# Kernel optimization log

Measured on AMD Instinct MI355X. Metric: run time of the kernel, lower is better.

Reference implementation:

```python
import jax, jax.numpy as jnp
import numpy as np

B, DC, DB, DF = 16384, 2048, 768, 256
NF = DB  # num_features (isSwinT=True)
EPS = 1e-5


def setup_inputs() -> dict:
    key = jax.random.key(0)
    ks = jax.random.split(key, 20)
    s = 0.02
    return {
        'x_context': jax.random.normal(ks[0], (B, DC), jnp.float32),
        'x_body': jax.random.normal(ks[1], (B, DB), jnp.float32),
        'x_face': jax.random.normal(ks[2], (B, DF), jnp.float32),
        'Wc': jax.random.normal(ks[3], (NF, DC), jnp.float32) * s,
        'bc': jax.random.normal(ks[4], (NF,), jnp.float32) * s,
        'Wa1': jax.random.normal(ks[5], (128, NF), jnp.float32) * s,
        'ba1': jax.random.normal(ks[6], (128,), jnp.float32) * s,
        'ga': jnp.ones((128,), jnp.float32),
        'bba': jnp.zeros((128,), jnp.float32),
        'Wa2': jax.random.normal(ks[7], (1, 128), jnp.float32) * s,
        'ba2': jax.random.normal(ks[8], (1,), jnp.float32) * s,
        'W1': jax.random.normal(ks[9], (256, NF * 3), jnp.float32) * s,
        'b1': jax.random.normal(ks[10], (256,), jnp.float32) * s,
        'g1': jnp.ones((256,), jnp.float32),
        'be1': jnp.zeros((256,), jnp.float32),
        'Wcat': jax.random.normal(ks[11], (26, 256), jnp.float32) * s,
        'bcat': jax.random.normal(ks[12], (26,), jnp.float32) * s,
    }


def _bn(x, g, b):
    # BatchNorm1d, training mode (biased batch stats), deterministic
    m = jnp.mean(x, axis=0)
    v = jnp.mean((x - m) ** 2, axis=0)
    return (x - m) * jax.lax.rsqrt(v + EPS) * g + b


def reference(x_context, x_body, x_face, Wc, bc, Wa1, ba1, ga, bba, Wa2, ba2,
              W1, b1, g1, be1, Wcat, bcat):
    # face repeated elementwise to body width: [B,256,1]->repeat(3)->view[B,768]
    face = jnp.repeat(x_face, DB // DF, axis=1)              # [B, NF]
    ctx = x_context @ Wc.T + bc                              # [B, NF]
    body = x_body                                            # [B, NF]

    def cross_atten(a, u, v):
        # two 1x1 dot-products, softmax over size-2 dim, weighted sum
        d = jnp.stack([jnp.sum(a * u, axis=1), jnp.sum(a * v, axis=1)], axis=1)  # [B,2]
        att = jax.nn.softmax(d, axis=1)
        # sum over dim2 of a[:, :, None] @ att[:, None, :] == a * att.sum(1)
        return a * jnp.sum(att, axis=1, keepdims=True)

    cfeat = cross_atten(ctx, body, face)
    bfeat = cross_atten(body, ctx, face)
    ffeat = cross_atten(face, ctx, body)

    def fc_att(x):
        h = _bn(x @ Wa1.T + ba1, ga, bba)
        h = jax.nn.gelu(h, approximate=False)
        return h @ Wa2.T + ba2                               # [B, 1]

    score = jax.nn.softmax(
        jnp.concatenate([fc_att(cfeat), fc_att(bfeat), fc_att(ffeat)], axis=1), axis=1)  # [B,3]
    cfeat = cfeat * score[:, 0:1]
    bfeat = bfeat * score[:, 1:2]
    ffeat = ffeat * score[:, 2:3]

    fuse = jnp.concatenate([cfeat, bfeat, ffeat], axis=1) @ W1.T + b1  # [B,256]
    fuse = jax.nn.relu(_bn(fuse, g1, be1))  # dropout p=0.5 treated as identity (eval)
    return fuse @ Wcat.T + bcat             # [B,26]
```

## Files before the change

### kernel.cpp

```cpp
#include <hip/hip_runtime.h>
#include <stdint.h>

typedef float f32x4 __attribute__((ext_vector_type(4)));
typedef short bf16x8 __attribute__((ext_vector_type(8)));
typedef unsigned short u16;

static constexpr int kB  = 16384;
static constexpr int kDC = 2048;
static constexpr int kNF = 768;
static constexpr float kEps = 1e-5f;

static constexpr size_t OFF_FEATS  = 0;
static constexpr size_t OFF_AXBF   = 75497472;
static constexpr size_t OFF_WCBF   = OFF_AXBF + 67108864;
static constexpr size_t OFF_WA1BF  = OFF_WCBF + 3145728;
static constexpr size_t OFF_W1BF   = OFF_WA1BF + 196608;
static constexpr size_t OFF_FUSE   = OFF_W1BF + 1179648;
static constexpr size_t OFF_SCORES = OFF_FUSE + 16777216;
static constexpr size_t OFF_STATS  = OFF_SCORES + 196608;

static __device__ __forceinline__ u16 f2bf(float x) {
  union { float f; unsigned u; } c; c.f = x;
  unsigned r = c.u + 0x7fffu + ((c.u >> 16) & 1u);
  return (u16)(r >> 16);
}

static __device__ __forceinline__ void cvt4(const float* __restrict__ in, u16* __restrict__ out, long v) {
  const float4 f = ((const float4*)in)[v];
  ((ushort4*)out)[v] = make_ushort4(f2bf(f.x), f2bf(f.y), f2bf(f.z), f2bf(f.w));
}

__global__ __launch_bounds__(256) void prep_kernel(
    const float* __restrict__ xc, const float* __restrict__ xb, const float* __restrict__ xf,
    const float* __restrict__ Wc, const float* __restrict__ Wa1, const float* __restrict__ W1,
    u16* __restrict__ axbf, u16* __restrict__ feats,
    u16* __restrict__ wcbf, u16* __restrict__ wa1bf, u16* __restrict__ w1bf)
{
  const int b = blockIdx.x, t = threadIdx.x;
  if (b < 1024) {
    const long base = (long)b * (32 * 256) + t;
#pragma unroll 8
    for (int i = 0; i < 32; ++i) cvt4(xc, axbf, base + (long)i * 256);
  } else if (b < 1536) {
    const long base = (long)(b - 1024) * (24 * 256) + t;
    u16* o = feats + (size_t)kB * kNF;
#pragma unroll 8
    for (int i = 0; i < 24; ++i) cvt4(xb, o, base + (long)i * 256);
  } else if (b < 1792) {
    const long base = (long)(b - 1536) * (16 * 256) + t;
#pragma unroll 4
    for (int i = 0; i < 16; ++i) {
      const long v = base + (long)i * 256;
      const float4 f = ((const float4*)xf)[v];
      u16 e0 = f2bf(f.x), e1 = f2bf(f.y), e2 = f2bf(f.z), e3 = f2bf(f.w);
      size_t p = (size_t)v * 4;
      size_t row = p >> 8;
      int col = (int)(p & 255);
      u16* o = feats + (size_t)2 * kB * kNF + row * kNF + col * 3;
      ushort4* o4 = (ushort4*)o;
      o4[0] = make_ushort4(e0, e0, e0, e1);
      o4[1] = make_ushort4(e1, e1, e2, e2);
      o4[2] = make_ushort4(e2, e3, e3, e3);
    }
  } else if (b < 1888) {
    const long base = (long)(b - 1792) * (16 * 256) + t;
#pragma unroll 8
    for (int i = 0; i < 16; ++i) cvt4(Wc, wcbf, base + (long)i * 256);
  } else if (b < 1896) {
    const long base = (long)(b - 1888) * (12 * 256) + t;
#pragma unroll 4
    for (int i = 0; i < 12; ++i) cvt4(Wa1, wa1bf, base + (long)i * 256);
  } else {
    const long base = (long)(b - 1896) * (18 * 256) + t;
#pragma unroll 6
    for (int i = 0; i < 18; ++i) cvt4(W1, w1bf, base + (long)i * 256);
  }
}

static __device__ __forceinline__ void gload16(const void* g, void* l) {
  __builtin_amdgcn_global_load_lds(
      (const __attribute__((address_space(1))) void*)g,
      (__attribute__((address_space(3))) void*)l, 16, 0, 0);
}

template <int OUT_BF16, int STATS>
__global__ __launch_bounds__(256) void gemm_bt(
    const u16* __restrict__ A, int lda, const u16* __restrict__ B, int ldb,
    const float* __restrict__ bias, void* __restrict__ Cv, int ldc, int K,
    float* __restrict__ stats)
{
  __shared__ __align__(16) u16 As[128 * 32];
  __shared__ __align__(16) u16 Bs[128 * 32];
  const int bx = blockIdx.x, by = blockIdx.y;
  const size_t m0 = (size_t)bx * 128;
  const int n0 = by * 128;
  const int t = threadIdx.x;
  const int lane = t & 63, wave = t >> 6;
  const int wm = (wave >> 1) * 64, wn = (wave & 1) * 64;
  const int fr = lane & 15, fq = lane >> 4;

  const int srow = t >> 2;
  const int scol = (t & 3) * 8;
  const u16* ga0 = A + (m0 + srow) * (size_t)lda + scol;
  const u16* ga1 = A + (m0 + 64 + srow) * (size_t)lda + scol;
  const u16* gb0 = B + (size_t)(n0 + srow) * ldb + scol;
  const u16* gb1 = B + (size_t)(n0 + 64 + srow) * ldb + scol;
  u16* la = As + t * 8;
  u16* lb = Bs + t * 8;
  const u16* fa = As + (wm + fr) * 32 + fq * 8;
  const u16* fb = Bs + (wn + fr) * 32 + fq * 8;

  f32x4 acc[4][4] = {};

  const int kt = K >> 5;
  for (int k = 0; k < kt; ++k) {
    __syncthreads();
    gload16(ga0, la);
    gload16(ga1, la + 2048);
    gload16(gb0, lb);
    gload16(gb1, lb + 2048);
    ga0 += 32; ga1 += 32; gb0 += 32; gb1 += 32;
    __syncthreads();
    bf16x8 av[4], bv[4];
#pragma unroll
    for (int mf = 0; mf < 4; ++mf) av[mf] = *(const bf16x8*)(fa + mf * 512);
#pragma unroll
    for (int nf = 0; nf < 4; ++nf) bv[nf] = *(const bf16x8*)(fb + nf * 512);
#pragma unroll
    for (int mf = 0; mf < 4; ++mf)
#pragma unroll
      for (int nf = 0; nf < 4; ++nf)
        acc[mf][nf] = __builtin_amdgcn_mfma_f32_16x16x32_bf16(av[mf], bv[nf], acc[mf][nf], 0, 0, 0);
  }

  float cs[4] = {}, cs2[4] = {};
#pragma unroll
  for (int mf = 0; mf < 4; ++mf) {
    const size_t rb = m0 + wm + mf * 16 + fq * 4;
#pragma unroll
    for (int nf = 0; nf < 4; ++nf) {
      const int gn = n0 + wn + nf * 16 + fr;
      const float bb = bias ? bias[gn] : 0.0f;
#pragma unroll
      for (int rr = 0; rr < 4; ++rr) {
        const float vv = acc[mf][nf][rr] + bb;
        if (OUT_BF16) ((u16*)Cv)[(rb + rr) * (size_t)ldc + gn] = f2bf(vv);
        else ((float*)Cv)[(rb + rr) * (size_t)ldc + gn] = vv;
        if (STATS) { cs[nf] += vv; cs2[nf] += vv * vv; }
      }
    }
  }
  if (STATS) {
    const int f = (int)(m0 >> 14);
#pragma unroll
    for (int nf = 0; nf < 4; ++nf) {
      float s = cs[nf], s2 = cs2[nf];
      s += __shfl_down(s, 32); s2 += __shfl_down(s2, 32);
      s += __shfl_down(s, 16); s2 += __shfl_down(s2, 16);
      if (fq == 0) {
        const int gn = n0 + wn + nf * 16 + fr;
        atomicAdd(&stats[(f * 128 + gn) * 2 + 0], s);
        atomicAdd(&stats[(f * 128 + gn) * 2 + 1], s2);
      }
    }
  }
}

__global__ __launch_bounds__(256, 2) void gemm_fuse(
    const u16* __restrict__ feats, const u16* __restrict__ w1,
    const float* __restrict__ scores, const float* __restrict__ b1,
    float* __restrict__ fuse, float* __restrict__ fstats)
{
  __shared__ __align__(16) u16 As[128 * 32];
  __shared__ __align__(16) u16 Bs[128 * 32];
  const int bx = blockIdx.x, by = blockIdx.y;
  const int m0 = bx * 128;
  const int n0 = by * 128;
  const int t = threadIdx.x;
  const int lane = t & 63, wave = t >> 6;
  const int wm = (wave >> 1) * 64, wn = (wave & 1) * 64;
  const int fr = lane & 15, fq = lane >> 4;
  const int srow = t >> 2;
  const int scol = (t & 3) * 8;
  u16* la = As + t * 8;
  u16* lb = Bs + t * 8;
  const u16* fa = As + (wm + fr) * 32 + fq * 8;
  const u16* fb = Bs + (wn + fr) * 32 + fq * 8;

  f32x4 tot[4][4] = {};

  for (int f = 0; f < 3; ++f) {
    const u16* ga0 = feats + (size_t)f * kB * kNF + (size_t)(m0 + srow) * kNF + scol;
    const u16* ga1 = ga0 + (size_t)64 * kNF;
    const u16* gb0 = w1 + f * kNF + (size_t)(n0 + srow) * (3 * kNF) + scol;
    const u16* gb1 = gb0 + (size_t)64 * (3 * kNF);

    f32x4 acc[4][4] = {};
    for (int k = 0; k < (kNF >> 5); ++k) {
      __syncthreads();
      gload16(ga0, la);
      gload16(ga1, la + 2048);
      gload16(gb0, lb);
      gload16(gb1, lb + 2048);
      ga0 += 32; ga1 += 32; gb0 += 32; gb1 += 32;
      __syncthreads();
      bf16x8 av[4], bv[4];
#pragma unroll
      for (int mf = 0; mf < 4; ++mf) av[mf] = *(const bf16x8*)(fa + mf * 512);
#pragma unroll
      for (int nf = 0; nf < 4; ++nf) bv[nf] = *(const bf16x8*)(fb + nf * 512);
#pragma unroll
      for (int mf = 0; mf < 4; ++mf)
#pragma unroll
        for (int nf = 0; nf < 4; ++nf)
          acc[mf][nf] = __builtin_amdgcn_mfma_f32_16x16x32_bf16(av[mf], bv[nf], acc[mf][nf], 0, 0, 0);
    }
#pragma unroll
    for (int mf = 0; mf < 4; ++mf) {
      const int rb = m0 + wm + mf * 16 + fq * 4;
#pragma unroll
      for (int rr = 0; rr < 4; ++rr) {
        const float sv = scores[(size_t)(rb + rr) * 3 + f];
#pragma unroll
        for (int nf = 0; nf < 4; ++nf) tot[mf][nf][rr] += sv * acc[mf][nf][rr];
      }
    }
  }

  float cs[4] = {}, cs2[4] = {};
#pragma unroll
  for (int mf = 0; mf < 4; ++mf) {
    const int rb = m0 + wm + mf * 16 + fq * 4;
#pragma unroll
    for (int nf = 0; nf < 4; ++nf) {
      const int gn = n0 + wn + nf * 16 + fr;
      const float bb = b1[gn];
#pragma unroll
      for (int rr = 0; rr < 4; ++rr) {
        const float vv = tot[mf][nf][rr] + bb;
        fuse[(size_t)(rb + rr) * 256 + gn] = vv;
        cs[nf] += vv; cs2[nf] += vv * vv;
      }
    }
  }
#pragma unroll
  for (int nf = 0; nf < 4; ++nf) {
    float s = cs[nf], s2 = cs2[nf];
    s += __shfl_down(s, 32); s2 += __shfl_down(s2, 32);
    s += __shfl_down(s, 16); s2 += __shfl_down(s2, 16);
    if (fq == 0) {
      const int gn = n0 + wn + nf * 16 + fr;
      atomicAdd(&fstats[gn * 2 + 0], s);
      atomicAdd(&fstats[gn * 2 + 1], s2);
    }
  }
}

__global__ __launch_bounds__(64) void att_kernel(
    const float* __restrict__ H, const float* __restrict__ stats,
    const float* __restrict__ ga, const float* __restrict__ bba,
    const float* __restrict__ Wa2, const float* __restrict__ ba2,
    float* __restrict__ scores)
{
  const int i = blockIdx.x, l = threadIdx.x;
  float d[3];
#pragma unroll
  for (int f = 0; f < 3; ++f) {
    float part = 0.f;
#pragma unroll
    for (int h = 0; h < 2; ++h) {
      const int c = l + h * 64;
      const float sum = stats[(f * 128 + c) * 2 + 0];
      const float sq  = stats[(f * 128 + c) * 2 + 1];
      const float m = sum * (1.f / kB);
      const float var = sq * (1.f / kB) - m * m;
      const float rs = rsqrtf(var + kEps);
      const float x = H[((size_t)f * kB + i) * 128 + c];
      const float xn = (x - m) * rs * ga[c] + bba[c];
      const float ge = 0.5f * xn * (1.f + erff(xn * 0.70710678118f));
      part += ge * Wa2[c];
    }
#pragma unroll
    for (int off = 32; off > 0; off >>= 1) part += __shfl_down(part, off);
    d[f] = part;
  }
  if (l == 0) {
    const float b2 = ba2[0];
    float d0 = d[0] + b2, d1 = d[1] + b2, d2 = d[2] + b2;
    const float mx = fmaxf(d0, fmaxf(d1, d2));
    const float e0 = expf(d0 - mx), e1 = expf(d1 - mx), e2 = expf(d2 - mx);
    const float inv = 1.f / (e0 + e1 + e2);
    scores[i * 3 + 0] = e0 * inv;
    scores[i * 3 + 1] = e1 * inv;
    scores[i * 3 + 2] = e2 * inv;
  }
}

__global__ __launch_bounds__(64) void final_kernel(
    const float* __restrict__ fuse, const float* __restrict__ fstats,
    const float* __restrict__ g1, const float* __restrict__ be1,
    const float* __restrict__ Wcat, const float* __restrict__ bcat,
    float* __restrict__ out)
{
  const int i = blockIdx.x, l = threadIdx.x;
  __shared__ float row[256];
#pragma unroll
  for (int h = 0; h < 4; ++h) {
    const int c = l + h * 64;
    const float sum = fstats[c * 2 + 0], sq = fstats[c * 2 + 1];
    const float m = sum * (1.f / kB);
    const float var = sq * (1.f / kB) - m * m;
    const float rs = rsqrtf(var + kEps);
    const float v = (fuse[(size_t)i * 256 + c] - m) * rs * g1[c] + be1[c];
    row[c] = fmaxf(v, 0.f);
  }
  __syncthreads();
  if (l < 26) {
    float acc = bcat[l];
    const float* w = Wcat + l * 256;
    for (int k2 = 0; k2 < 256; ++k2) acc += row[k2] * w[k2];
    out[(size_t)i * 26 + l] = acc;
  }
}

extern "C" void kernel_launch(void* const* d_in, const int* in_sizes, int n_in,
                              void* d_out, int out_size, void* d_ws, size_t ws_size,
                              hipStream_t stream) {
  (void)in_sizes; (void)n_in; (void)out_size; (void)ws_size;
  const float* xc   = (const float*)d_in[0];
  const float* xb   = (const float*)d_in[1];
  const float* xf   = (const float*)d_in[2];
  const float* Wc   = (const float*)d_in[3];
  const float* bc   = (const float*)d_in[4];
  const float* Wa1  = (const float*)d_in[5];
  const float* ba1  = (const float*)d_in[6];
  const float* ga   = (const float*)d_in[7];
  const float* bba  = (const float*)d_in[8];
  const float* Wa2  = (const float*)d_in[9];
  const float* ba2  = (const float*)d_in[10];
  const float* W1   = (const float*)d_in[11];
  const float* b1   = (const float*)d_in[12];
  const float* g1   = (const float*)d_in[13];
  const float* be1  = (const float*)d_in[14];
  const float* Wcat = (const float*)d_in[15];
  const float* bcat = (const float*)d_in[16];
  float* out = (float*)d_out;

  char* ws = (char*)d_ws;
  u16* feats   = (u16*)(ws + OFF_FEATS);
  u16* axbf    = (u16*)(ws + OFF_AXBF);
  float* H     = (float*)(ws + OFF_AXBF);
  u16* wcbf    = (u16*)(ws + OFF_WCBF);
  u16* wa1bf   = (u16*)(ws + OFF_WA1BF);
  u16* w1bf    = (u16*)(ws + OFF_W1BF);
  float* fuse  = (float*)(ws + OFF_FUSE);
  float* scores= (float*)(ws + OFF_SCORES);
  float* hst   = (float*)(ws + OFF_STATS);
  float* fst   = (float*)(ws + OFF_STATS + 3072);

  hipMemsetAsync(ws + OFF_STATS, 0, 5120, stream);
  prep_kernel<<<1928, 256, 0, stream>>>(xc, xb, xf, Wc, Wa1, W1, axbf, feats, wcbf, wa1bf, w1bf);
  gemm_bt<1, 0><<<dim3(128, 6), 256, 0, stream>>>(axbf, kDC, wcbf, kDC, bc, feats, kNF, kDC, nullptr);
  gemm_bt<0, 1><<<dim3(384, 1), 256, 0, stream>>>(feats, kNF, wa1bf, kNF, ba1, H, 128, kNF, hst);
  att_kernel<<<kB, 64, 0, stream>>>(H, hst, ga, bba, Wa2, ba2, scores);
  gemm_fuse<<<dim3(128, 2), 256, 0, stream>>>(feats, w1bf, scores, b1, fuse, fst);
  final_kernel<<<kB, 64, 0, stream>>>(fuse, fst, g1, be1, Wcat, bcat, out);
}
```

Before: 330.0 us.

## Fuse fp32-to-bf16 conversion of x_context into GEMM and shrink M tiles

The context GEMM now reads fp32 x_context directly, converting it to bf16 in registers with a one-step register prefetch and writing it to LDS. This removes the separate prep pass that wrote and re-read a 64MB bf16 copy. The attention-hidden GEMM and the fuse GEMM switch from 128-row to 64-row M tiles to launch twice as many blocks, which trades weight-tile reuse for parallelism. Prep blocks are also resized to 4 vectors per thread.

```diff
diff --git a/kernel.cpp b/kernel.cpp
--- a/kernel.cpp
+++ b/kernel.cpp
@@ -1,4 +1,5 @@
 #include <hip/hip_runtime.h>
+#include <hip/hip_bf16.h>
 #include <stdint.h>
 
 typedef float f32x4 __attribute__((ext_vector_type(4)));
@@ -11,8 +12,8 @@
 static constexpr float kEps = 1e-5f;
 
 static constexpr size_t OFF_FEATS  = 0;
-static constexpr size_t OFF_AXBF   = 75497472;
-static constexpr size_t OFF_WCBF   = OFF_AXBF + 67108864;
+static constexpr size_t OFF_X      = 75497472;
+static constexpr size_t OFF_WCBF   = OFF_X + 67108864;
 static constexpr size_t OFF_WA1BF  = OFF_WCBF + 3145728;
 static constexpr size_t OFF_W1BF   = OFF_WA1BF + 196608;
 static constexpr size_t OFF_FUSE   = OFF_W1BF + 1179648;
@@ -25,32 +26,33 @@
   return (u16)(r >> 16);
 }
 
+static __device__ __forceinline__ unsigned pk2(float lo, float hi) {
+  union { __hip_bfloat162 h; unsigned u; } c;
+  c.h = __float22bfloat162_rn(make_float2(lo, hi));
+  return c.u;
+}
+
 static __device__ __forceinline__ void cvt4(const float* __restrict__ in, u16* __restrict__ out, long v) {
   const float4 f = ((const float4*)in)[v];
   ((ushort4*)out)[v] = make_ushort4(f2bf(f.x), f2bf(f.y), f2bf(f.z), f2bf(f.w));
 }
 
 __global__ __launch_bounds__(256) void prep_kernel(
-    const float* __restrict__ xc, const float* __restrict__ xb, const float* __restrict__ xf,
+    const float* __restrict__ xb, const float* __restrict__ xf,
     const float* __restrict__ Wc, const float* __restrict__ Wa1, const float* __restrict__ W1,
-    u16* __restrict__ axbf, u16* __restrict__ feats,
-    u16* __restrict__ wcbf, u16* __restrict__ wa1bf, u16* __restrict__ w1bf)
+    u16* __restrict__ feats, u16* __restrict__ wcbf, u16* __restrict__ wa1bf, u16* __restrict__ w1bf)
 {
   const int b = blockIdx.x, t = threadIdx.x;
-  if (b < 1024) {
-    const long base = (long)b * (32 * 256) + t;
-#pragma unroll 8
-    for (int i = 0; i < 32; ++i) cvt4(xc, axbf, base + (long)i * 256);
-  } else if (b < 1536) {
-    const long base = (long)(b - 1024) * (24 * 256) + t;
+  if (b < 3072) {
+    const long base = (long)b * 1024 + t;
     u16* o = feats + (size_t)kB * kNF;
-#pragma unroll 8
-    for (int i = 0; i < 24; ++i) cvt4(xb, o, base + (long)i * 256);
-  } else if (b < 1792) {
-    const long base = (long)(b - 1536) * (16 * 256) + t;
-#pragma unroll 4
-    for (int i = 0; i < 16; ++i) {
-      const long v = base + (long)i * 256;
+#pragma unroll
+    for (int i = 0; i < 4; ++i) cvt4(xb, o, base + i * 256);
+  } else if (b < 4096) {
+    const long base = (long)(b - 3072) * 1024 + t;
+#pragma unroll
+    for (int i = 0; i < 4; ++i) {
+      const long v = base + i * 256;
       const float4 f = ((const float4*)xf)[v];
       u16 e0 = f2bf(f.x), e1 = f2bf(f.y), e2 = f2bf(f.z), e3 = f2bf(f.w);
       size_t p = (size_t)v * 4;
@@ -62,18 +64,18 @@
       o4[1] = make_ushort4(e1, e1, e2, e2);
       o4[2] = make_ushort4(e2, e3, e3, e3);
     }
-  } else if (b < 1888) {
-    const long base = (long)(b - 1792) * (16 * 256) + t;
-#pragma unroll 8
-    for (int i = 0; i < 16; ++i) cvt4(Wc, wcbf, base + (long)i * 256);
-  } else if (b < 1896) {
-    const long base = (long)(b - 1888) * (12 * 256) + t;
-#pragma unroll 4
-    for (int i = 0; i < 12; ++i) cvt4(Wa1, wa1bf, base + (long)i * 256);
+  } else if (b < 4480) {
+    const long base = (long)(b - 4096) * 1024 + t;
+#pragma unroll
+    for (int i = 0; i < 4; ++i) cvt4(Wc, wcbf, base + i * 256);
+  } else if (b < 4504) {
+    const long base = (long)(b - 4480) * 1024 + t;
+#pragma unroll
+    for (int i = 0; i < 4; ++i) cvt4(Wa1, wa1bf, base + i * 256);
   } else {
-    const long base = (long)(b - 1896) * (18 * 256) + t;
-#pragma unroll 6
-    for (int i = 0; i < 18; ++i) cvt4(W1, w1bf, base + (long)i * 256);
+    const long base = (long)(b - 4504) * 1024 + t;
+#pragma unroll
+    for (int i = 0; i < 4; ++i) cvt4(W1, w1bf, base + i * 256);
   }
 }
 
@@ -83,11 +85,9 @@
       (__attribute__((address_space(3))) void*)l, 16, 0, 0);
 }
 
-template <int OUT_BF16, int STATS>
-__global__ __launch_bounds__(256) void gemm_bt(
-    const u16* __restrict__ A, int lda, const u16* __restrict__ B, int ldb,
-    const float* __restrict__ bias, void* __restrict__ Cv, int ldc, int K,
-    float* __restrict__ stats)
+__global__ __launch_bounds__(256) void gemm_a32(
+    const float* __restrict__ A, const u16* __restrict__ B,
+    const float* __restrict__ bias, u16* __restrict__ C)
 {
   __shared__ __align__(16) u16 As[128 * 32];
   __shared__ __align__(16) u16 Bs[128 * 32];
@@ -99,53 +99,125 @@
   const int wm = (wave >> 1) * 64, wn = (wave & 1) * 64;
   const int fr = lane & 15, fq = lane >> 4;
 
-  const int srow = t >> 2;
-  const int scol = (t & 3) * 8;
+  const int srow = t >> 2, scol = (t & 3) * 8;
+  const u16* gb0 = B + (size_t)(n0 + srow) * kDC + scol;
+  const u16* gb1 = B + (size_t)(n0 + 64 + srow) * kDC + scol;
+  u16* lb = Bs + t * 8;
+
+  const int arow = t >> 1, acol = (t & 1) * 16;
+  const float* ga = A + (m0 + arow) * (size_t)kDC + acol;
+  u16* lawr = As + arow * 32 + acol;
+
+  const u16* fa = As + (wm + fr) * 32 + fq * 8;
+  const u16* fb = Bs + (wn + fr) * 32 + fq * 8;
+
+  f32x4 acc[4][4] = {};
+  float4 ra0 = ((const float4*)ga)[0], ra1 = ((const float4*)ga)[1],
+         ra2 = ((const float4*)ga)[2], ra3 = ((const float4*)ga)[3];
+
+  for (int k = 0; k < 64; ++k) {
+    __syncthreads();
+    gload16(gb0, lb);
+    gload16(gb1, lb + 2048);
+    gb0 += 32; gb1 += 32;
+    uint4 w0, w1;
+    w0.x = pk2(ra0.x, ra0.y); w0.y = pk2(ra0.z, ra0.w);
+    w0.z = pk2(ra1.x, ra1.y); w0.w = pk2(ra1.z, ra1.w);
+    w1.x = pk2(ra2.x, ra2.y); w1.y = pk2(ra2.z, ra2.w);
+    w1.z = pk2(ra3.x, ra3.y); w1.w = pk2(ra3.z, ra3.w);
+    ((uint4*)lawr)[0] = w0;
+    ((uint4*)(lawr + 8))[0] = w1;
+    if (k < 63) {
+      ga += 32;
+      ra0 = ((const float4*)ga)[0]; ra1 = ((const float4*)ga)[1];
+      ra2 = ((const float4*)ga)[2]; ra3 = ((const float4*)ga)[3];
+    }
+    __syncthreads();
+    bf16x8 av[4], bv[4];
+#pragma unroll
+    for (int mf = 0; mf < 4; ++mf) av[mf] = *(const bf16x8*)(fa + mf * 512);
+#pragma unroll
+    for (int nf = 0; nf < 4; ++nf) bv[nf] = *(const bf16x8*)(fb + nf * 512);
+#pragma unroll
+    for (int mf = 0; mf < 4; ++mf)
+#pragma unroll
+      for (int nf = 0; nf < 4; ++nf)
+        acc[mf][nf] = __builtin_amdgcn_mfma_f32_16x16x32_bf16(av[mf], bv[nf], acc[mf][nf], 0, 0, 0);
+  }
+
+#pragma unroll
+  for (int mf = 0; mf < 4; ++mf) {
+    const size_t rb = m0 + wm + mf * 16 + fq * 4;
+#pragma unroll
+    for (int nf = 0; nf < 4; ++nf) {
+      const int gn = n0 + wn + nf * 16 + fr;
+      const float bb = bias[gn];
+#pragma unroll
+      for (int rr = 0; rr < 4; ++rr)
+        C[(rb + rr) * (size_t)kNF + gn] = f2bf(acc[mf][nf][rr] + bb);
+    }
+  }
+}
+
+template <int STATS>
+__global__ __launch_bounds__(256) void gemm_bt64(
+    const u16* __restrict__ A, int lda, const u16* __restrict__ B, int ldb,
+    const float* __restrict__ bias, float* __restrict__ C, int ldc, int K,
+    float* __restrict__ stats)
+{
+  __shared__ __align__(16) u16 As[64 * 32];
+  __shared__ __align__(16) u16 Bs[128 * 32];
+  const int bx = blockIdx.x, by = blockIdx.y;
+  const size_t m0 = (size_t)bx * 64;
+  const int n0 = by * 128;
+  const int t = threadIdx.x;
+  const int lane = t & 63, wave = t >> 6;
+  const int wn = wave * 32;
+  const int fr = lane & 15, fq = lane >> 4;
+
+  const int srow = t >> 2, scol = (t & 3) * 8;
   const u16* ga0 = A + (m0 + srow) * (size_t)lda + scol;
-  const u16* ga1 = A + (m0 + 64 + srow) * (size_t)lda + scol;
   const u16* gb0 = B + (size_t)(n0 + srow) * ldb + scol;
   const u16* gb1 = B + (size_t)(n0 + 64 + srow) * ldb + scol;
   u16* la = As + t * 8;
   u16* lb = Bs + t * 8;
-  const u16* fa = As + (wm + fr) * 32 + fq * 8;
+  const u16* fa = As + fr * 32 + fq * 8;
   const u16* fb = Bs + (wn + fr) * 32 + fq * 8;
 
-  f32x4 acc[4][4] = {};
+  f32x4 acc[4][2] = {};
 
   const int kt = K >> 5;
   for (int k = 0; k < kt; ++k) {
     __syncthreads();
     gload16(ga0, la);
-    gload16(ga1, la + 2048);
     gload16(gb0, lb);
     gload16(gb1, lb + 2048);
-    ga0 += 32; ga1 += 32; gb0 += 32; gb1 += 32;
+    ga0 += 32; gb0 += 32; gb1 += 32;
     __syncthreads();
-    bf16x8 av[4], bv[4];
+    bf16x8 av[4], bv[2];
 #pragma unroll
     for (int mf = 0; mf < 4; ++mf) av[mf] = *(const bf16x8*)(fa + mf * 512);
 #pragma unroll
-    for (int nf = 0; nf < 4; ++nf) bv[nf] = *(const bf16x8*)(fb + nf * 512);
+    for (int nf = 0; nf < 2; ++nf) bv[nf] = *(const bf16x8*)(fb + nf * 512);
 #pragma unroll
     for (int mf = 0; mf < 4; ++mf)
 #pragma unroll
-      for (int nf = 0; nf < 4; ++nf)
+      for (int nf = 0; nf < 2; ++nf)
         acc[mf][nf] = __builtin_amdgcn_mfma_f32_16x16x32_bf16(av[mf], bv[nf], acc[mf][nf], 0, 0, 0);
   }
 
-  float cs[4] = {}, cs2[4] = {};
+  float cs[2] = {}, cs2[2] = {};
 #pragma unroll
   for (int mf = 0; mf < 4; ++mf) {
-    const size_t rb = m0 + wm + mf * 16 + fq * 4;
-#pragma unroll
-    for (int nf = 0; nf < 4; ++nf) {
+    const size_t rb = m0 + mf * 16 + fq * 4;
+#pragma unroll
+    for (int nf = 0; nf < 2; ++nf) {
       const int gn = n0 + wn + nf * 16 + fr;
-      const float bb = bias ? bias[gn] : 0.0f;
+      const float bb = bias[gn];
 #pragma unroll
       for (int rr = 0; rr < 4; ++rr) {
         const float vv = acc[mf][nf][rr] + bb;
-        if (OUT_BF16) ((u16*)Cv)[(rb + rr) * (size_t)ldc + gn] = f2bf(vv);
-        else ((float*)Cv)[(rb + rr) * (size_t)ldc + gn] = vv;
+        C[(rb + rr) * (size_t)ldc + gn] = vv;
         if (STATS) { cs[nf] += vv; cs2[nf] += vv * vv; }
       }
     }
@@ -153,7 +225,7 @@
   if (STATS) {
     const int f = (int)(m0 >> 14);
 #pragma unroll
-    for (int nf = 0; nf < 4; ++nf) {
+    for (int nf = 0; nf < 2; ++nf) {
       float s = cs[nf], s2 = cs2[nf];
       s += __shfl_down(s, 32); s2 += __shfl_down(s2, 32);
       s += __shfl_down(s, 16); s2 += __shfl_down(s2, 16);
@@ -166,85 +238,82 @@
   }
 }
 
-__global__ __launch_bounds__(256, 2) void gemm_fuse(
+__global__ __launch_bounds__(256) void gemm_fuse64(
     const u16* __restrict__ feats, const u16* __restrict__ w1,
     const float* __restrict__ scores, const float* __restrict__ b1,
     float* __restrict__ fuse, float* __restrict__ fstats)
 {
-  __shared__ __align__(16) u16 As[128 * 32];
+  __shared__ __align__(16) u16 As[64 * 32];
   __shared__ __align__(16) u16 Bs[128 * 32];
   const int bx = blockIdx.x, by = blockIdx.y;
-  const int m0 = bx * 128;
+  const size_t m0 = (size_t)bx * 64;
   const int n0 = by * 128;
   const int t = threadIdx.x;
   const int lane = t & 63, wave = t >> 6;
-  const int wm = (wave >> 1) * 64, wn = (wave & 1) * 64;
+  const int wn = wave * 32;
   const int fr = lane & 15, fq = lane >> 4;
-  const int srow = t >> 2;
-  const int scol = (t & 3) * 8;
+  const int srow = t >> 2, scol = (t & 3) * 8;
   u16* la = As + t * 8;
   u16* lb = Bs + t * 8;
-  const u16* fa = As + (wm + fr) * 32 + fq * 8;
+  const u16* fa = As + fr * 32 + fq * 8;
   const u16* fb = Bs + (wn + fr) * 32 + fq * 8;
 
-  f32x4 tot[4][4] = {};
+  f32x4 tot[4][2] = {};
 
   for (int f = 0; f < 3; ++f) {
-    const u16* ga0 = feats + (size_t)f * kB * kNF + (size_t)(m0 + srow) * kNF + scol;
-    const u16* ga1 = ga0 + (size_t)64 * kNF;
+    const u16* ga0 = feats + (size_t)f * kB * kNF + (m0 + srow) * (size_t)kNF + scol;
     const u16* gb0 = w1 + f * kNF + (size_t)(n0 + srow) * (3 * kNF) + scol;
     const u16* gb1 = gb0 + (size_t)64 * (3 * kNF);
 
-    f32x4 acc[4][4] = {};
+    f32x4 acc[4][2] = {};
     for (int k = 0; k < (kNF >> 5); ++k) {
       __syncthreads();
       gload16(ga0, la);
-      gload16(ga1, la + 2048);
       gload16(gb0, lb);
       gload16(gb1, lb + 2048);
-      ga0 += 32; ga1 += 32; gb0 += 32; gb1 += 32;
+      ga0 += 32; gb0 += 32; gb1 += 32;
       __syncthreads();
-      bf16x8 av[4], bv[4];
+      bf16x8 av[4], bv[2];
 #pragma unroll
       for (int mf = 0; mf < 4; ++mf) av[mf] = *(const bf16x8*)(fa + mf * 512);
 #pragma unroll
-      for (int nf = 0; nf < 4; ++nf) bv[nf] = *(const bf16x8*)(fb + nf * 512);
+      for (int nf = 0; nf < 2; ++nf) bv[nf] = *(const bf16x8*)(fb + nf * 512);
 #pragma unroll
       for (int mf = 0; mf < 4; ++mf)
 #pragma unroll
-        for (int nf = 0; nf < 4; ++nf)
+        for (int nf = 0; nf < 2; ++nf)
           acc[mf][nf] = __builtin_amdgcn_mfma_f32_16x16x32_bf16(av[mf], bv[nf], acc[mf][nf], 0, 0, 0);
     }
 #pragma unroll
     for (int mf = 0; mf < 4; ++mf) {
-      const int rb = m0 + wm + mf * 16 + fq * 4;
+      const size_t rb = m0 + mf * 16 + fq * 4;
 #pragma unroll
       for (int rr = 0; rr < 4; ++rr) {
-        const float sv = scores[(size_t)(rb + rr) * 3 + f];
-#pragma unroll
-        for (int nf = 0; nf < 4; ++nf) tot[mf][nf][rr] += sv * acc[mf][nf][rr];
+        const float sv = scores[(rb + rr) * 3 + f];
+#pragma unroll
+        for (int nf = 0; nf < 2; ++nf) tot[mf][nf][rr] += sv * acc[mf][nf][rr];
       }
     }
   }
 
-  float cs[4] = {}, cs2[4] = {};
+  float cs[2] = {}, cs2[2] = {};
 #pragma unroll
   for (int mf = 0; mf < 4; ++mf) {
-    const int rb = m0 + wm + mf * 16 + fq * 4;
-#pragma unroll
-    for (int nf = 0; nf < 4; ++nf) {
+    const size_t rb = m0 + mf * 16 + fq * 4;
+#pragma unroll
+    for (int nf = 0; nf < 2; ++nf) {
       const int gn = n0 + wn + nf * 16 + fr;
       const float bb = b1[gn];
 #pragma unroll
       for (int rr = 0; rr < 4; ++rr) {
         const float vv = tot[mf][nf][rr] + bb;
-        fuse[(size_t)(rb + rr) * 256 + gn] = vv;
+        fuse[(rb + rr) * 256 + gn] = vv;
         cs[nf] += vv; cs2[nf] += vv * vv;
       }
     }
   }
 #pragma unroll
-  for (int nf = 0; nf < 4; ++nf) {
+  for (int nf = 0; nf < 2; ++nf) {
     float s = cs[nf], s2 = cs2[nf];
     s += __shfl_down(s, 32); s2 += __shfl_down(s2, 32);
     s += __shfl_down(s, 16); s2 += __shfl_down(s2, 16);
@@ -348,8 +417,7 @@
 
   char* ws = (char*)d_ws;
   u16* feats   = (u16*)(ws + OFF_FEATS);
-  u16* axbf    = (u16*)(ws + OFF_AXBF);
-  float* H     = (float*)(ws + OFF_AXBF);
+  float* H     = (float*)(ws + OFF_X);
   u16* wcbf    = (u16*)(ws + OFF_WCBF);
   u16* wa1bf   = (u16*)(ws + OFF_WA1BF);
   u16* w1bf    = (u16*)(ws + OFF_W1BF);
@@ -359,10 +427,10 @@
   float* fst   = (float*)(ws + OFF_STATS + 3072);
 
   hipMemsetAsync(ws + OFF_STATS, 0, 5120, stream);
-  prep_kernel<<<1928, 256, 0, stream>>>(xc, xb, xf, Wc, Wa1, W1, axbf, feats, wcbf, wa1bf, w1bf);
-  gemm_bt<1, 0><<<dim3(128, 6), 256, 0, stream>>>(axbf, kDC, wcbf, kDC, bc, feats, kNF, kDC, nullptr);
-  gemm_bt<0, 1><<<dim3(384, 1), 256, 0, stream>>>(feats, kNF, wa1bf, kNF, ba1, H, 128, kNF, hst);
+  prep_kernel<<<4648, 256, 0, stream>>>(xb, xf, Wc, Wa1, W1, feats, wcbf, wa1bf, w1bf);
+  gemm_a32<<<dim3(128, 6), 256, 0, stream>>>(xc, wcbf, bc, feats);
+  gemm_bt64<1><<<dim3(768, 1), 256, 0, stream>>>(feats, kNF, wa1bf, kNF, ba1, H, 128, kNF, hst);
   att_kernel<<<kB, 64, 0, stream>>>(H, hst, ga, bba, Wa2, ba2, scores);
-  gemm_fuse<<<dim3(128, 2), 256, 0, stream>>>(feats, w1bf, scores, b1, fuse, fst);
+  gemm_fuse64<<<dim3(256, 2), 256, 0, stream>>>(feats, w1bf, scores, b1, fuse, fst);
   final_kernel<<<kB, 64, 0, stream>>>(fuse, fst, g1, be1, Wcat, bcat, out);
 }
```

Result: faster. 292.2 us (-11.5%).
